# Kernel optimization log

Measured on AMD Instinct MI355X. Metric: run time of the kernel, lower is better.

The kernel has to match this reference:

```python
import jax, jax.numpy as jnp
import numpy as np

N = 50000      # nodes
E = 800000     # edges (avg degree 16)
IN = 64        # in_features (upper layer dim)
OUT = 32       # out_features
STEPS = 20     # n_inference_steps
LR = 0.1       # inference_lr
SLOPE = 0.2    # LeakyReLU negative slope


def setup_inputs() -> dict:
    key = jax.random.key(0)
    k1, k2, k3, k4 = jax.random.split(key, 4)
    mu_upper = jax.random.normal(k1, (N, IN), dtype=jnp.float32)
    # xavier-uniform-like scale for W [OUT, IN] and a [2*OUT]
    lim_w = float(np.sqrt(6.0 / (IN + OUT)))
    W = jax.random.uniform(k2, (OUT, IN), jnp.float32, -lim_w, lim_w)
    lim_a = float(np.sqrt(6.0 / (1 + 2 * OUT)))
    a = jax.random.uniform(k3, (2 * OUT,), jnp.float32, -lim_a, lim_a)
    edge_index = jax.random.randint(k4, (2, E), 0, N, dtype=jnp.int32)
    return {"mu_upper": mu_upper, "W": W, "a": a, "edge_index": edge_index}


def _segment_softmax(scores, dst, n_nodes):
    # numerically stable softmax grouped by destination node
    m = jax.ops.segment_max(scores, dst, num_segments=n_nodes)
    m = jnp.where(jnp.isfinite(m), m, 0.0)  # mirrors nan_to_num on -inf fill
    e = jnp.exp(scores - m[dst])
    s = jax.ops.segment_sum(e, dst, num_segments=n_nodes)
    return e / (s[dst] + 1e-8)


def reference(mu_upper, W, a, edge_index):
    src, dst = edge_index[0], edge_index[1]
    n_nodes = mu_upper.shape[0]
    out_f = W.shape[0]
    # W @ mu_upper is invariant over the inference loop
    transformed = mu_upper @ W.T                       # [N, OUT]
    a_src, a_dst = a[:out_f], a[out_f:]

    # uniform 1/degree initial attention
    deg = jax.ops.segment_sum(jnp.ones((src.shape[0],), jnp.float32), dst,
                              num_segments=n_nodes)
    alpha0 = 1.0 / (deg[dst] + 1e-8)                   # [E]
    mu0 = jnp.zeros((n_nodes, out_f), jnp.float32)

    def top_down(alpha):
        msgs = alpha[:, None] * transformed[src]       # [E, OUT]
        agg = jax.ops.segment_sum(msgs, dst, num_segments=n_nodes)
        return jax.nn.relu(agg)

    def step(carry, _):
        mu, alpha = carry
        mu_hat = top_down(alpha)
        errors = mu - mu_hat
        # a^T [err_src || err_dst] == err_src@a[:OUT] + err_dst@a[OUT:]
        scores = errors @ a_src
        scores = scores[src] + (errors @ a_dst)[dst]   # [E]
        scores = jnp.where(scores > 0, scores, SLOPE * scores)  # LeakyReLU
        alpha_new = _segment_softmax(scores, dst, n_nodes)
        mu_new = mu - LR * errors                      # inference step (no lower layer)
        return (mu_new, alpha_new), None

    (mu, alpha), _ = jax.lax.scan(step, (mu0, alpha0), None, length=STEPS)
    mu_hat = top_down(alpha)
    errors = mu - mu_hat
    return mu, errors, alpha
```

## Files before the change

kernel.cpp:

```cpp
#include <hip/hip_runtime.h>
#include <hip/hip_fp16.h>
#include <math.h>

#define N_NODES 50000
#define N_EDGES 800000
#define IN_F 64
#define OUT_F 32
#define STEPS 20
#define LR 0.1f
#define SLOPE 0.2f
#define PAD 64
#define IT_NBLK 2048
#define NODES_PER_PASS (IT_NBLK * 8)


__global__ void csr_build_pad(const int* __restrict__ src, const int* __restrict__ dst,
                              int* __restrict__ cursor, int* __restrict__ csr_pad,
                              int* __restrict__ perm) {
    int e = blockIdx.x * blockDim.x + threadIdx.x;
    if (e < N_EDGES) {
        int d = dst[e];
        int p = atomicAdd(&cursor[d], 1);
        int slot = (d << 6) + p;
        csr_pad[slot] = src[e];
        perm[e] = slot;
    }
}

__global__ __launch_bounds__(256) void transform_kernel(const float* __restrict__ mu_upper,
                                                        const float* __restrict__ W,
                                                        __half* __restrict__ th) {
    __shared__ float4 Ws[OUT_F][17];
    int tid = threadIdx.x;
    for (int t = tid; t < OUT_F * 16; t += 256) Ws[t >> 4][t & 15] = ((const float4*)W)[t];
    __syncthreads();
    int t = blockIdx.x * 256 + tid;
    if (t >= N_NODES * 16) return;
    int n = t >> 4, op = t & 15;
    const float4* m4 = (const float4*)(mu_upper + n * IN_F);
    float a0 = 0.f, a1 = 0.f;
#pragma unroll
    for (int k = 0; k < 16; k++) {
        float4 r = m4[k];
        float4 x = Ws[2 * op][k];
        a0 += r.x * x.x + r.y * x.y + r.z * x.z + r.w * x.w;
        float4 y = Ws[2 * op + 1][k];
        a1 += r.x * y.x + r.y * y.y + r.z * y.z + r.w * y.w;
    }
    *(__half2*)(th + n * OUT_F + 2 * op) = __floats2half2_rn(a0, a1);
}

__device__ __forceinline__ void fma_h8(uint2 u, float al, float4& agg) {
    float2 f01 = __half22float2(*(__half2*)&u.x);
    float2 f23 = __half22float2(*(__half2*)&u.y);
    agg.x = fmaf(al, f01.x, agg.x);
    agg.y = fmaf(al, f01.y, agg.y);
    agg.z = fmaf(al, f23.x, agg.z);
    agg.w = fmaf(al, f23.y, agg.w);
}


__global__ __launch_bounds__(256) void firstA_nb(
        const int* __restrict__ deg, const int* __restrict__ csr_pad,
        const __half* __restrict__ th,
        float* __restrict__ mu, const float* __restrict__ a_vec,
        float* __restrict__ s_out_src, float* __restrict__ s_out_dst) {
    int lane = threadIdx.x & 63;
    int lane32 = lane & 31;
    int po = ((threadIdx.x >> 6) << 1) + (lane >> 5);
    int eslot = lane32 >> 3, c = lane32 & 7;
    for (int nb = blockIdx.x * 8; nb < N_NODES; nb += NODES_PER_PASS) {
        int n = nb + po;
        if (n >= N_NODES) break;
        int cnt = deg[n];
        int rs = n << 6;
        int my_src = (lane32 < cnt) ? csr_pad[rs + lane32] : 0;
        float4 agg = make_float4(0.f, 0.f, 0.f, 0.f);
        int lim = cnt < 32 ? cnt : 32;
        int kmax = (lim + 3) >> 2;
        for (int k = 0; k < kmax; k++) {
            int sl = eslot + 4 * k;
            int sj = __shfl(my_src, sl, 32);
            if (sl < lim) {
                uint2 u = *(const uint2*)(th + (sj << 5) + (c << 2));
                fma_h8(u, 1.0f, agg);
            }
        }
        for (int j = rs + 32 + eslot; j < rs + cnt; j += 4) {
            uint2 u = *(const uint2*)(th + (csr_pad[j] << 5) + (c << 2));
            fma_h8(u, 1.0f, agg);
        }
#pragma unroll
        for (int off = 8; off <= 16; off <<= 1) {
            agg.x += __shfl_xor(agg.x, off, 32);
            agg.y += __shfl_xor(agg.y, off, 32);
            agg.z += __shfl_xor(agg.z, off, 32);
            agg.w += __shfl_xor(agg.w, off, 32);
        }
        if (eslot == 0) {
            float al0 = 1.0f / ((float)cnt + 1e-8f);
            float4 mh;
            mh.x = fmaxf(al0 * agg.x, 0.f);
            mh.y = fmaxf(al0 * agg.y, 0.f);
            mh.z = fmaxf(al0 * agg.z, 0.f);
            mh.w = fmaxf(al0 * agg.w, 0.f);
            float4 err = make_float4(-mh.x, -mh.y, -mh.z, -mh.w);
            float4 nm = make_float4(LR * mh.x, LR * mh.y, LR * mh.z, LR * mh.w);
            *(float4*)(mu + (n << 5) + (c << 2)) = nm;
            float4 as = *(const float4*)(a_vec + (c << 2));
            float4 ad = *(const float4*)(a_vec + OUT_F + (c << 2));
            float v1 = err.x * as.x + err.y * as.y + err.z * as.z + err.w * as.w;
            float v2 = err.x * ad.x + err.y * ad.y + err.z * ad.z + err.w * ad.w;
#pragma unroll
            for (int off = 1; off <= 4; off <<= 1) {
                v1 += __shfl_xor(v1, off, 32);
                v2 += __shfl_xor(v2, off, 32);
            }
            if (c == 0) { s_out_src[n] = v1; s_out_dst[n] = v2; }
        }
    }
}

template <bool FINAL>
__global__ __launch_bounds__(256) void fused_nb(
        const int* __restrict__ deg, const int* __restrict__ csr_pad,
        const __half* __restrict__ th,
        float* __restrict__ mu, float* __restrict__ errors_out,
        const float* __restrict__ a_vec,
        const float* __restrict__ s_in_src, const float* __restrict__ s_in_dst,
        float* __restrict__ s_out_src, float* __restrict__ s_out_dst,
        float* __restrict__ alpha_pad) {
    int lane = threadIdx.x & 63;
    int lane32 = lane & 31;
    int po = ((threadIdx.x >> 6) << 1) + (lane >> 5);
    int eslot = lane32 >> 3, c = lane32 & 7;
    for (int nb = blockIdx.x * 8; nb < N_NODES; nb += NODES_PER_PASS) {
        int n = nb + po;
        if (n >= N_NODES) break;
        int cnt = deg[n];
        int rs = n << 6;
        float sd = s_in_dst[n];
        int my_src = (lane32 < cnt) ? csr_pad[rs + lane32] : 0;
        float e0 = 0.f;
        if (lane32 < cnt) {
            float v = s_in_src[my_src] + sd;
            v = v > 0.f ? v : SLOPE * v;
            e0 = __expf(v);
        }
        float ssum = e0;
        for (int j2 = rs + 32 + lane32; j2 < rs + cnt; j2 += 32) {
            float v = s_in_src[csr_pad[j2]] + sd;
            v = v > 0.f ? v : SLOPE * v;
            ssum += __expf(v);
        }
#pragma unroll
        for (int off = 1; off <= 16; off <<= 1) ssum += __shfl_xor(ssum, off, 32);
        float inv = 1.0f / (ssum + 1e-8f);
        float my_alpha = e0 * inv;
        if (FINAL) {
            if (lane32 < cnt) alpha_pad[rs + lane32] = my_alpha;
            for (int j2 = rs + 32 + lane32; j2 < rs + cnt; j2 += 32) {
                float v = s_in_src[csr_pad[j2]] + sd;
                v = v > 0.f ? v : SLOPE * v;
                alpha_pad[j2] = __expf(v) * inv;
            }
        }
        float4 agg = make_float4(0.f, 0.f, 0.f, 0.f);
        int lim = cnt < 32 ? cnt : 32;
        int kmax = (lim + 3) >> 2;
        for (int k = 0; k < kmax; k++) {
            int sl = eslot + 4 * k;
            float al = __shfl(my_alpha, sl, 32);
            int sj = __shfl(my_src, sl, 32);
            if (sl < lim) {
                uint2 u = *(const uint2*)(th + (sj << 5) + (c << 2));
                fma_h8(u, al, agg);
            }
        }
        for (int j = rs + 32 + eslot; j < rs + cnt; j += 4) {
            int sj = csr_pad[j];
            float v = s_in_src[sj] + sd;
            v = v > 0.f ? v : SLOPE * v;
            float al = __expf(v) * inv;
            uint2 u = *(const uint2*)(th + (sj << 5) + (c << 2));
            fma_h8(u, al, agg);
        }
#pragma unroll
        for (int off = 8; off <= 16; off <<= 1) {
            agg.x += __shfl_xor(agg.x, off, 32);
            agg.y += __shfl_xor(agg.y, off, 32);
            agg.z += __shfl_xor(agg.z, off, 32);
            agg.w += __shfl_xor(agg.w, off, 32);
        }
        if (eslot == 0) {
            float4* mup = (float4*)(mu + (n << 5) + (c << 2));
            float4 muv = *mup;
            float4 err;
            err.x = muv.x - fmaxf(agg.x, 0.f);
            err.y = muv.y - fmaxf(agg.y, 0.f);
            err.z = muv.z - fmaxf(agg.z, 0.f);
            err.w = muv.w - fmaxf(agg.w, 0.f);
            if (FINAL) {
                *(float4*)(errors_out + (n << 5) + (c << 2)) = err;
            } else {
                float4 nm;
                nm.x = fmaf(-LR, err.x, muv.x);
                nm.y = fmaf(-LR, err.y, muv.y);
                nm.z = fmaf(-LR, err.z, muv.z);
                nm.w = fmaf(-LR, err.w, muv.w);
                *mup = nm;
                float4 as = *(const float4*)(a_vec + (c << 2));
                float4 ad = *(const float4*)(a_vec + OUT_F + (c << 2));
                float v1 = err.x * as.x + err.y * as.y + err.z * as.z + err.w * as.w;
                float v2 = err.x * ad.x + err.y * ad.y + err.z * ad.z + err.w * ad.w;
#pragma unroll
                for (int off = 1; off <= 4; off <<= 1) {
                    v1 += __shfl_xor(v1, off, 32);
                    v2 += __shfl_xor(v2, off, 32);
                }
                if (c == 0) { s_out_src[n] = v1; s_out_dst[n] = v2; }
            }
        }
    }
}

__global__ void gather_alpha_kernel(const int* __restrict__ perm,
                                    const float* __restrict__ alpha_pad,
                                    float* __restrict__ alpha_out) {
    for (int e = blockIdx.x * blockDim.x + threadIdx.x; e < N_EDGES;
         e += IT_NBLK * 256) {
        alpha_out[e] = alpha_pad[perm[e]];
    }
}

extern "C" void kernel_launch(void* const* d_in, const int* in_sizes, int n_in,
                              void* d_out, int out_size, void* d_ws, size_t ws_size,
                              hipStream_t stream) {
    const float* mu_upper = (const float*)d_in[0];
    const float* W        = (const float*)d_in[1];
    const float* a_vec    = (const float*)d_in[2];
    const int*   edge_idx = (const int*)d_in[3];
    const int*   src = edge_idx;
    const int*   dst = edge_idx + N_EDGES;

    float* out = (float*)d_out;
    float* mu         = out;
    float* errors_out = out + N_NODES * OUT_F;
    float* alpha_out  = out + 2 * N_NODES * OUT_F;

    char* ws = (char*)d_ws;
    int*   cursor    = (int*)(ws + 0);
    float* sA        = (float*)(ws + 200064);
    float* sB        = (float*)(ws + 400064);
    float* sAd       = (float*)(ws + 600064);
    float* sBd       = (float*)(ws + 800064);
    int*   perm      = (int*)(ws + 1000064);
    __half* th       = (__half*)(ws + 4200064);
    int*   csr_pad   = (int*)(ws + 7400064);
    float* alpha_pad = (float*)(ws + 20200064);

    hipMemsetAsync(cursor, 0, N_NODES * sizeof(int), stream);

    csr_build_pad<<<(N_EDGES + 255) / 256, 256, 0, stream>>>(src, dst, cursor, csr_pad, perm);
    transform_kernel<<<(N_NODES * 16 + 255) / 256, 256, 0, stream>>>(mu_upper, W, th);

    firstA_nb<<<IT_NBLK, 256, 0, stream>>>(cursor, csr_pad, th, mu, a_vec, sA, sAd);
    float *si = sA, *sid = sAd, *so = sB, *sod = sBd;
    for (int t = 2; t <= STEPS; t++) {
        fused_nb<false><<<IT_NBLK, 256, 0, stream>>>(cursor, csr_pad, th, mu, errors_out,
                                                     a_vec, si, sid, so, sod, alpha_pad);
        float* tmp;
        tmp = si; si = so; so = tmp;
        tmp = sid; sid = sod; sod = tmp;
    }
    fused_nb<true><<<IT_NBLK, 256, 0, stream>>>(cursor, csr_pad, th, mu, errors_out,
                                                a_vec, si, sid, so, sod, alpha_pad);
    gather_alpha_kernel<<<IT_NBLK, 256, 0, stream>>>(perm, alpha_pad, alpha_out);
}
```

Before: 518.8 us.

## Recompute final alpha per edge from node softmax stats instead of permuted scatter

The final step no longer writes per-edge alpha into a padded CSR buffer and gathers it back through a permutation array. It stores each destination's score term and inverse softmax sum, and a final edge-order kernel recomputes alpha from the source score plus those stats. This drops the perm writes in CSR build and the padded alpha scatter/gather traffic, at the cost of recomputing exp per edge. The first-32-edge loop is also fully unrolled to a fixed 8 iterations, guarded per slot.

```diff
diff --git a/kernel.cpp b/kernel.cpp
--- a/kernel.cpp
+++ b/kernel.cpp
@@ -9,21 +9,17 @@
 #define STEPS 20
 #define LR 0.1f
 #define SLOPE 0.2f
-#define PAD 64
 #define IT_NBLK 2048
 #define NODES_PER_PASS (IT_NBLK * 8)
 
 
 __global__ void csr_build_pad(const int* __restrict__ src, const int* __restrict__ dst,
-                              int* __restrict__ cursor, int* __restrict__ csr_pad,
-                              int* __restrict__ perm) {
+                              int* __restrict__ cursor, int* __restrict__ csr_pad) {
     int e = blockIdx.x * blockDim.x + threadIdx.x;
     if (e < N_EDGES) {
         int d = dst[e];
         int p = atomicAdd(&cursor[d], 1);
-        int slot = (d << 6) + p;
-        csr_pad[slot] = src[e];
-        perm[e] = slot;
+        csr_pad[(d << 6) + p] = src[e];
     }
 }
 
@@ -77,8 +73,8 @@
         int my_src = (lane32 < cnt) ? csr_pad[rs + lane32] : 0;
         float4 agg = make_float4(0.f, 0.f, 0.f, 0.f);
         int lim = cnt < 32 ? cnt : 32;
-        int kmax = (lim + 3) >> 2;
-        for (int k = 0; k < kmax; k++) {
+#pragma unroll
+        for (int k = 0; k < 8; k++) {
             int sl = eslot + 4 * k;
             int sj = __shfl(my_src, sl, 32);
             if (sl < lim) {
@@ -129,7 +125,7 @@
         const float* __restrict__ a_vec,
         const float* __restrict__ s_in_src, const float* __restrict__ s_in_dst,
         float* __restrict__ s_out_src, float* __restrict__ s_out_dst,
-        float* __restrict__ alpha_pad) {
+        float2* __restrict__ dinv) {
     int lane = threadIdx.x & 63;
     int lane32 = lane & 31;
     int po = ((threadIdx.x >> 6) << 1) + (lane >> 5);
@@ -157,18 +153,10 @@
         for (int off = 1; off <= 16; off <<= 1) ssum += __shfl_xor(ssum, off, 32);
         float inv = 1.0f / (ssum + 1e-8f);
         float my_alpha = e0 * inv;
-        if (FINAL) {
-            if (lane32 < cnt) alpha_pad[rs + lane32] = my_alpha;
-            for (int j2 = rs + 32 + lane32; j2 < rs + cnt; j2 += 32) {
-                float v = s_in_src[csr_pad[j2]] + sd;
-                v = v > 0.f ? v : SLOPE * v;
-                alpha_pad[j2] = __expf(v) * inv;
-            }
-        }
         float4 agg = make_float4(0.f, 0.f, 0.f, 0.f);
         int lim = cnt < 32 ? cnt : 32;
-        int kmax = (lim + 3) >> 2;
-        for (int k = 0; k < kmax; k++) {
+#pragma unroll
+        for (int k = 0; k < 8; k++) {
             int sl = eslot + 4 * k;
             float al = __shfl(my_alpha, sl, 32);
             int sj = __shfl(my_src, sl, 32);
@@ -202,6 +190,7 @@
             err.w = muv.w - fmaxf(agg.w, 0.f);
             if (FINAL) {
                 *(float4*)(errors_out + (n << 5) + (c << 2)) = err;
+                if (c == 0) dinv[n] = make_float2(sd, inv);
             } else {
                 float4 nm;
                 nm.x = fmaf(-LR, err.x, muv.x);
@@ -224,12 +213,16 @@
     }
 }
 
-__global__ void gather_alpha_kernel(const int* __restrict__ perm,
-                                    const float* __restrict__ alpha_pad,
-                                    float* __restrict__ alpha_out) {
+__global__ void alpha_final_kernel(const int* __restrict__ src, const int* __restrict__ dst,
+                                   const float* __restrict__ s_src,
+                                   const float2* __restrict__ dinv,
+                                   float* __restrict__ alpha_out) {
     for (int e = blockIdx.x * blockDim.x + threadIdx.x; e < N_EDGES;
          e += IT_NBLK * 256) {
-        alpha_out[e] = alpha_pad[perm[e]];
+        float2 di = dinv[dst[e]];
+        float v = s_src[src[e]] + di.x;
+        v = v > 0.f ? v : SLOPE * v;
+        alpha_out[e] = __expf(v) * di.y;
     }
 }
 
@@ -249,31 +242,30 @@
     float* alpha_out  = out + 2 * N_NODES * OUT_F;
 
     char* ws = (char*)d_ws;
-    int*   cursor    = (int*)(ws + 0);
-    float* sA        = (float*)(ws + 200064);
-    float* sB        = (float*)(ws + 400064);
-    float* sAd       = (float*)(ws + 600064);
-    float* sBd       = (float*)(ws + 800064);
-    int*   perm      = (int*)(ws + 1000064);
-    __half* th       = (__half*)(ws + 4200064);
-    int*   csr_pad   = (int*)(ws + 7400064);
-    float* alpha_pad = (float*)(ws + 20200064);
+    int*    cursor = (int*)(ws + 0);
+    float*  sA     = (float*)(ws + 200064);
+    float*  sB     = (float*)(ws + 400064);
+    float*  sAd    = (float*)(ws + 600064);
+    float*  sBd    = (float*)(ws + 800064);
+    float2* dinv   = (float2*)(ws + 1000064);
+    __half* th     = (__half*)(ws + 1400064);
+    int*   csr_pad = (int*)(ws + 4600064);
 
     hipMemsetAsync(cursor, 0, N_NODES * sizeof(int), stream);
 
-    csr_build_pad<<<(N_EDGES + 255) / 256, 256, 0, stream>>>(src, dst, cursor, csr_pad, perm);
+    csr_build_pad<<<(N_EDGES + 255) / 256, 256, 0, stream>>>(src, dst, cursor, csr_pad);
     transform_kernel<<<(N_NODES * 16 + 255) / 256, 256, 0, stream>>>(mu_upper, W, th);
 
     firstA_nb<<<IT_NBLK, 256, 0, stream>>>(cursor, csr_pad, th, mu, a_vec, sA, sAd);
     float *si = sA, *sid = sAd, *so = sB, *sod = sBd;
     for (int t = 2; t <= STEPS; t++) {
         fused_nb<false><<<IT_NBLK, 256, 0, stream>>>(cursor, csr_pad, th, mu, errors_out,
-                                                     a_vec, si, sid, so, sod, alpha_pad);
+                                                     a_vec, si, sid, so, sod, dinv);
         float* tmp;
         tmp = si; si = so; so = tmp;
         tmp = sid; sid = sod; sod = tmp;
     }
     fused_nb<true><<<IT_NBLK, 256, 0, stream>>>(cursor, csr_pad, th, mu, errors_out,
-                                                a_vec, si, sid, so, sod, alpha_pad);
-    gather_alpha_kernel<<<IT_NBLK, 256, 0, stream>>>(perm, alpha_pad, alpha_out);
-}
+                                                a_vec, si, sid, so, sod, dinv);
+    alpha_final_kernel<<<IT_NBLK, 256, 0, stream>>>(src, dst, si, dinv, alpha_out);
+}
```

New measurement: 506.9 us. 2.3% less time.
